# Kernel optimization log

Measured on AMD Instinct MI355X. Metric: run time of the kernel, lower is better.

The kernel has to match this reference:

```python
import jax, jax.numpy as jnp
import numpy as np

B, S, HID = 2, 2048, 2048
H, HKV, D = 16, 4, 128        # num_heads, num_kv_heads, head_dim
G = H // HKV                   # GQA group size
CLIP = 8.0                     # clip_qkv
THETA = 10000.0                # rope_theta_within_seq
N_SEQS = 8                     # max_num_sequences


def setup_inputs() -> dict:
    key = jax.random.key(0)
    ks = jax.random.split(key, 6)
    hidden_states = jax.random.normal(ks[0], (B, S, HID), dtype=jnp.float32)
    within_seq_position_ids = jnp.broadcast_to(jnp.arange(S, dtype=jnp.int64), (B, S))
    global_position_ids = jnp.broadcast_to(jnp.arange(S, dtype=jnp.int64), (B, S))
    sequence_ids = jnp.sort(jax.random.randint(ks[1], (B, S), 0, N_SEQS, dtype=jnp.int64), axis=-1)
    scale = 0.02
    Wq = jax.random.normal(ks[2], (H * D, HID), dtype=jnp.float32) * scale
    Wk = jax.random.normal(ks[3], (HKV * D, HID), dtype=jnp.float32) * scale
    Wv = jax.random.normal(ks[4], (HKV * D, HID), dtype=jnp.float32) * scale
    Wo = jax.random.normal(ks[5], (HID, H * D), dtype=jnp.float32) * scale
    return {"hidden_states": hidden_states,
            "within_seq_position_ids": within_seq_position_ids,
            "global_position_ids": global_position_ids,
            "sequence_ids": sequence_ids,
            "Wq": Wq, "Wk": Wk, "Wv": Wv, "Wo": Wo}


def _rotate_half(x):
    x1, x2 = jnp.split(x, 2, axis=-1)
    return jnp.concatenate((-x2, x1), axis=-1)


def _rope_cos_sin(position_ids, dtype):
    # inv_freq: [D/2]
    inv_freq = THETA ** (-(jnp.arange(0, D, 2, dtype=jnp.float32) / D))
    angles = position_ids.astype(jnp.float32)[..., None] * inv_freq  # [B,S,D/2]
    angles = jnp.concatenate((angles, angles), axis=-1)              # [B,S,D]
    # unsqueeze head dim -> [B,S,1,D]
    return jnp.cos(angles)[:, :, None, :].astype(dtype), jnp.sin(angles)[:, :, None, :].astype(dtype)


def reference(hidden_states, within_seq_position_ids, global_position_ids, sequence_ids, Wq, Wk, Wv, Wo):
    b, s, _ = hidden_states.shape
    q = (hidden_states @ Wq.T).reshape(b, s, H, D)
    k = (hidden_states @ Wk.T).reshape(b, s, HKV, D)
    v = (hidden_states @ Wv.T).reshape(b, s, HKV, D)
    # clip_qkv
    q = jnp.clip(q, -CLIP, CLIP)
    k = jnp.clip(k, -CLIP, CLIP)
    v = jnp.clip(v, -CLIP, CLIP)
    # RoPE (within_seq layer -> within_seq_position_ids)
    cos, sin = _rope_cos_sin(within_seq_position_ids, q.dtype)
    q = q * cos + _rotate_half(q) * sin
    k = k * cos + _rotate_half(k) * sin
    # GQA: group queries by kv head instead of materializing repeat_kv
    q = q.transpose(0, 2, 1, 3).reshape(b, HKV, G, s, D)  # [B,HKV,G,S,D]
    k = k.transpose(0, 2, 1, 3)                            # [B,HKV,S,D]
    v = v.transpose(0, 2, 1, 3)
    scores = jnp.einsum('bhgqd,bhkd->bhgqk', q, k) / jnp.sqrt(jnp.asarray(D, q.dtype))
    # block-diagonal (same sequence) causal mask
    qi = jnp.arange(s)
    causal = qi[:, None] >= qi[None, :]                    # [S,S]
    same_seq = sequence_ids[:, :, None] == sequence_ids[:, None, :]  # [B,S,S]
    mask = (causal[None] & same_seq)[:, None, None, :, :]  # [B,1,1,S,S]
    scores = jnp.where(mask, scores, jnp.finfo(scores.dtype).min)
    attn = jax.nn.softmax(scores, axis=-1)
    out = jnp.einsum('bhgqk,bhkd->bhgqd', attn, v)         # [B,HKV,G,S,D]
    out = out.reshape(b, H, s, D).transpose(0, 2, 1, 3).reshape(b, s, H * D)
    return out @ Wo.T
```

## Files before the change

### kernel.cpp

```cpp
#include <hip/hip_runtime.h>
#include <hip/hip_bf16.h>

typedef __hip_bfloat16 bf16;
typedef __attribute__((ext_vector_type(8))) short bf16x8;
typedef __attribute__((ext_vector_type(4))) float f32x4;

#define MFMA_BF16(a, b, c) __builtin_amdgcn_mfma_f32_16x16x32_bf16((a), (b), (c), 0, 0, 0)

#define B_   2
#define S_   2048
#define HID_ 2048
#define H_   16
#define HKV_ 4
#define D_   128

#define GLOAD_LDS(gptr, lptr) \
  __builtin_amdgcn_global_load_lds((const __attribute__((address_space(1))) void*)(gptr), \
                                   (__attribute__((address_space(3))) void*)(lptr), 16, 0, 0)

template <int N>
__device__ __forceinline__ void vmw() {
  if constexpr (N == 0)      asm volatile("s_waitcnt vmcnt(0)" ::: "memory");
  else if constexpr (N == 4) asm volatile("s_waitcnt vmcnt(4)" ::: "memory");
  else if constexpr (N == 5) asm volatile("s_waitcnt vmcnt(5)" ::: "memory");
  else                       asm volatile("s_waitcnt vmcnt(6)" ::: "memory");
}

__device__ __forceinline__ void blk_barrier() {
  __builtin_amdgcn_sched_barrier(0);
  __builtin_amdgcn_s_barrier();
  __builtin_amdgcn_sched_barrier(0);
}

__global__ void cvt_all(const float* __restrict__ hidden, const float* __restrict__ Wq,
                        const float* __restrict__ Wk, const float* __restrict__ Wv,
                        const float* __restrict__ Wo,
                        bf16* __restrict__ Xb, bf16* __restrict__ Wqkv, bf16* __restrict__ Wob) {
  long long i4 = (long long)blockIdx.x * 256 + threadIdx.x;
  const float* src; bf16* dst; long long off;
  if (i4 < 2097152)      { src = hidden; dst = Xb;             off = i4; }
  else if (i4 < 3145728) { src = Wq;     dst = Wqkv;           off = i4 - 2097152; }
  else if (i4 < 3407872) { src = Wk;     dst = Wqkv + 4194304; off = i4 - 3145728; }
  else if (i4 < 3670016) { src = Wv;     dst = Wqkv + 5242880; off = i4 - 3407872; }
  else                   { src = Wo;     dst = Wob;            off = i4 - 3670016; }
  float4 v = *reinterpret_cast<const float4*>(src + off * 4);
  alignas(8) bf16 t[4];
  t[0] = __float2bfloat16(v.x);
  t[1] = __float2bfloat16(v.y);
  t[2] = __float2bfloat16(v.z);
  t[3] = __float2bfloat16(v.w);
  *reinterpret_cast<short4*>(dst + off * 4) = *reinterpret_cast<const short4*>(t);
}

__global__ void seq_start(const int* __restrict__ seq, int* __restrict__ sstart) {
  int t = blockIdx.x * 256 + threadIdx.x;
  int b = t >> 11, s = t & (S_ - 1);
  const int* sb = seq + b * S_;
  int sid = sb[s];
  int lo = 0, hi = s;
  while (lo < hi) {
    int mid = (lo + hi) >> 1;
    if (sb[mid] < sid) lo = mid + 1; else hi = mid;
  }
  sstart[t] = lo;
}

template <int BM, int BN, int OUT_BF16>
__global__ __launch_bounds__(512, 2) void gemm8p(const bf16* __restrict__ A,
                                                 const bf16* __restrict__ Bw,
                                                 void* __restrict__ Cout,
                                                 int M, int N, int K) {
  constexpr int MR = BM / 32;
  constexpr int NR = BN / 64;
  constexpr int LA = BM / 128;
  constexpr int QD = NR + 2;

  __shared__ bf16 As[2][2][BM * 32];
  __shared__ bf16 Bs[2][BN * 64];

  const int tid  = threadIdx.x;
  const int lane = tid & 63;
  const int w    = tid >> 6;
  const int wr   = w >> 2;
  const int wc   = w & 3;
  const int ln15 = lane & 15, g = lane >> 4;

  const int nwg = gridDim.x;
  int bid = blockIdx.x;
  bid = (bid & 7) * (nwg >> 3) + (bid >> 3);
  const int nbn = N / BN;
  const int m0 = (bid / nbn) * BM;
  const int n0 = (bid % nbn) * BN;

  f32x4 acc[MR][NR] = {};

  auto stageA = [&](int db, int kh, int t) {
    int kc = t * 64 + kh * 32;
#pragma unroll
    for (int r = 0; r < LA; r++) {
      int sIdx = r * 512 + tid;
      int row = sIdx >> 2;
      int ss = (sIdx & 3) ^ ((row >> 1) & 3);
      GLOAD_LDS(A + (size_t)(m0 + row) * K + kc + ss * 8, &As[db][kh][(r * 512 + w * 64) * 8]);
    }
  };
  auto stageB = [&](int db, int t) {
#pragma unroll
    for (int r = 0; r < NR; r++) {
      int sIdx = r * 512 + tid;
      int row = sIdx >> 3;
      int cs = (sIdx & 7) ^ (row & 7);
      GLOAD_LDS(Bw + (size_t)(n0 + row) * K + t * 64 + cs * 8, &Bs[db][(size_t)(r * 512 + w * 64) * 8]);
    }
  };

  bf16x8 af[4], bfr[NR];
  auto rdA = [&](int db, int kh, int mb) {
#pragma unroll
    for (int m = 0; m < 4; m++) {
      int row = wr * (BM / 2) + (mb + m) * 16 + ln15;
      af[m] = *reinterpret_cast<const bf16x8*>(&As[db][kh][row * 32 + ((g ^ ((row >> 1) & 3)) << 3)]);
    }
  };
  auto rdB = [&](int db, int kh) {
#pragma unroll
    for (int n = 0; n < NR; n++) {
      int row = wc * (BN / 4) + n * 16 + ln15;
      int sl = ((kh << 2) + g) ^ (row & 7);
      bfr[n] = *reinterpret_cast<const bf16x8*>(&Bs[db][row * 64 + sl * 8]);
    }
  };
  auto MF = [&](int mb) {
    __builtin_amdgcn_s_setprio(1);
#pragma unroll
    for (int m = 0; m < 4; m++)
#pragma unroll
      for (int n = 0; n < NR; n++)
        acc[mb + m][n] = MFMA_BF16(af[m], bfr[n], acc[mb + m][n]);
    __builtin_amdgcn_s_setprio(0);
  };

  const int NT = K >> 6;

  stageA(0, 0, 0);
  stageA(0, 1, 0);
  stageB(0, 0);
  stageA(1, 0, 1);
  stageB(1, 1);
  vmw<QD>();
  blk_barrier();

  for (int T = 0; T < NT; ++T) {
    const int db = T & 1, dn = db ^ 1;

    rdA(db, 0, 0); rdB(db, 0);
    if (T + 1 < NT) stageA(dn, 1, T + 1);
    blk_barrier(); MF(0); blk_barrier();
    rdA(db, 0, 4);
    blk_barrier(); MF(4); blk_barrier();
    rdA(db, 1, 0); rdB(db, 1);
    if (T + 2 < NT) stageA(db, 0, T + 2);
    blk_barrier(); MF(0); blk_barrier();
    rdA(db, 1, 4);
    if (T + 2 < NT) stageB(db, T + 2);
    if (T + 1 < NT) {
      if (T == NT - 2) vmw<0>(); else vmw<QD>();
    }
    blk_barrier(); MF(4); blk_barrier();
  }

#pragma unroll
  for (int m = 0; m < MR; m++)
#pragma unroll
    for (int n = 0; n < NR; n++)
#pragma unroll
      for (int r = 0; r < 4; r++) {
        int row = m0 + wr * (BM / 2) + m * 16 + g * 4 + r;
        int col = n0 + wc * (BN / 4) + n * 16 + ln15;
        if constexpr (OUT_BF16) {
          ((bf16*)Cout)[(size_t)row * N + col] = __float2bfloat16(acc[m][n][r]);
        } else {
          ((float*)Cout)[(size_t)row * N + col] = acc[m][n][r];
        }
      }
}

__global__ __launch_bounds__(256) void qkv_post(const bf16* __restrict__ QKV,
                                                const int* __restrict__ wpos,
                                                bf16* __restrict__ Qs,
                                                bf16* __restrict__ Ks,
                                                bf16* __restrict__ Vt) {
  const int row = blockIdx.x;
  const int b = row >> 11, s = row & (S_ - 1);
  const int t = threadIdx.x;
  const bf16* R = QKV + (size_t)row * 3072;
  const float pos = (float)wpos[row];
  const float kln = 0.14391156831212787f;
  const float qscale = 0.08838834764831845f;

  for (int p = t; p < 1024; p += 256) {
    int h = p >> 6, i = p & 63;
    float ang = pos * expf(-(float)i * kln);
    float sn, cs;
    sincosf(ang, &sn, &cs);
    float x1 = __bfloat162float(R[h * 128 + i]);
    float x2 = __bfloat162float(R[h * 128 + 64 + i]);
    x1 = fminf(fmaxf(x1, -8.f), 8.f);
    x2 = fminf(fmaxf(x2, -8.f), 8.f);
    float y1 = (x1 * cs - x2 * sn) * qscale;
    float y2 = (x2 * cs + x1 * sn) * qscale;
    size_t qb = ((size_t)(b * H_ + h) * S_ + s) * D_;
    Qs[qb + i]      = __float2bfloat16(y1);
    Qs[qb + 64 + i] = __float2bfloat16(y2);
  }
  {
    int kh = t >> 6, i = t & 63;
    float ang = pos * expf(-(float)i * kln);
    float sn, cs;
    sincosf(ang, &sn, &cs);
    float x1 = __bfloat162float(R[2048 + kh * 128 + i]);
    float x2 = __bfloat162float(R[2048 + kh * 128 + 64 + i]);
    x1 = fminf(fmaxf(x1, -8.f), 8.f);
    x2 = fminf(fmaxf(x2, -8.f), 8.f);
    float y1 = x1 * cs - x2 * sn;
    float y2 = x2 * cs + x1 * sn;
    size_t kb = ((size_t)(b * HKV_ + kh) * S_ + s) * D_;
    Ks[kb + i]      = __float2bfloat16(y1);
    Ks[kb + 64 + i] = __float2bfloat16(y2);
  }
  for (int e = t; e < 512; e += 256) {
    int kh = e >> 7, d = e & 127;
    float x = __bfloat162float(R[2560 + e]);
    x = fminf(fmaxf(x, -8.f), 8.f);
    Vt[((size_t)(b * HKV_ + kh) * D_ + d) * S_ + s] = __float2bfloat16(x);
  }
}

__global__ __launch_bounds__(256) void attn_fwd(const bf16* __restrict__ Qs,
                                                const bf16* __restrict__ Ks,
                                                const bf16* __restrict__ Vt,
                                                const int* __restrict__ sstart,
                                                bf16* __restrict__ att) {
  __shared__ bf16 Kl[2][32 * 128];
  __shared__ bf16 Vl[2][128 * 32];
  __shared__ bf16 Plds[4][16 * 32];

  const int tid = threadIdx.x;
  const int lane = tid & 63, w = tid >> 6;
  const int ln15 = lane & 15, g = lane >> 4;

  const int wg = ((blockIdx.x & 7) << 7) | (blockIdx.x >> 3);
  const int qt  = wg & 127;
  const int kvh = (wg >> 7) & 3;
  const int b   = wg >> 9;
  const int h   = kvh * 4 + w;
  const int q0  = qt * 16;
  const int qi  = q0 + ln15;

  const bf16* Qrow = Qs + ((size_t)(b * H_ + h) * S_ + qi) * D_;
  bf16x8 qf[4];
#pragma unroll
  for (int c = 0; c < 4; c++)
    qf[c] = *reinterpret_cast<const bf16x8*>(Qrow + c * 32 + g * 8);

  const int sQ = sstart[b * S_ + qi];
  const int kstart = __builtin_amdgcn_readfirstlane(__shfl(sQ, 0));
  const int kend = q0 + 15;

  const bf16* Kb = Ks + (size_t)(b * HKV_ + kvh) * S_ * D_;
  const bf16* Vb = Vt + (size_t)(b * HKV_ + kvh) * D_ * S_;

  auto stage = [&](int buf, int kb) {
#pragma unroll
    for (int p = 0; p < 2; p++) {
      int slot = p * 256 + tid;
      int row = slot >> 4;
      int cs = (slot & 15) ^ (row & 15);
      int gr = min(kb + row, S_ - 1);
      GLOAD_LDS(Kb + (size_t)gr * D_ + cs * 8, &Kl[buf][(p * 256 + w * 64) * 8]);
    }
#pragma unroll
    for (int p = 0; p < 2; p++) {
      int slot = p * 256 + tid;
      int d = slot >> 2, c = slot & 3;
      int cs = c ^ (d & 3);
      int gcol = min(kb + cs * 8, S_ - 8);
      GLOAD_LDS(Vb + (size_t)d * S_ + gcol, &Vl[buf][(p * 256 + w * 64) * 8]);
    }
  };

  float m = -1e30f, lsum = 0.f;
  f32x4 o[8] = {};

  stage(0, kstart);
  int buf = 0;
  for (int kb = kstart; kb <= kend; kb += 32) {
    __syncthreads();
    if (kb + 32 <= kend) stage(buf ^ 1, kb + 32);

    bf16x8 kf0[4], kf1[4];
#pragma unroll
    for (int c = 0; c < 4; c++) {
      kf0[c] = *reinterpret_cast<const bf16x8*>(&Kl[buf][ln15 * 128 + (((c * 4 + g) ^ ln15) << 3)]);
      kf1[c] = *reinterpret_cast<const bf16x8*>(&Kl[buf][(16 + ln15) * 128 + (((c * 4 + g) ^ ln15) << 3)]);
    }
    f32x4 s0 = {0.f, 0.f, 0.f, 0.f}, s1 = {0.f, 0.f, 0.f, 0.f};
#pragma unroll
    for (int c = 0; c < 4; c++) {
      s0 = MFMA_BF16(kf0[c], qf[c], s0);
      s1 = MFMA_BF16(kf1[c], qf[c], s1);
    }

    float sc[8];
    float tmax = -1e30f;
#pragma unroll
    for (int r = 0; r < 4; r++) {
      int k0i = kb + g * 4 + r;
      int k1i = k0i + 16;
      float x0 = (k0i >= sQ && k0i <= qi) ? s0[r] : -1e30f;
      float x1 = (k1i >= sQ && k1i <= qi) ? s1[r] : -1e30f;
      sc[r] = x0;
      sc[4 + r] = x1;
      tmax = fmaxf(tmax, fmaxf(x0, x1));
    }
    tmax = fmaxf(tmax, __shfl_xor(tmax, 16));
    tmax = fmaxf(tmax, __shfl_xor(tmax, 32));
    float mn  = fmaxf(m, tmax);
    float fac = __expf(m - mn);
    float ps = 0.f;
    alignas(16) bf16 pb[8];
#pragma unroll
    for (int i2 = 0; i2 < 8; i2++) {
      float p = (sc[i2] < -1e29f) ? 0.f : __expf(sc[i2] - mn);
      ps += p;
      pb[i2] = __float2bfloat16(p);
    }
    ps += __shfl_xor(ps, 16);
    ps += __shfl_xor(ps, 32);
    lsum = lsum * fac + ps;
    m = mn;
#pragma unroll
    for (int t2 = 0; t2 < 8; t2++) o[t2] *= fac;

    *reinterpret_cast<short4*>(&Plds[w][ln15 * 32 + g * 4])      = *reinterpret_cast<const short4*>(&pb[0]);
    *reinterpret_cast<short4*>(&Plds[w][ln15 * 32 + 16 + g * 4]) = *reinterpret_cast<const short4*>(&pb[4]);
    __builtin_amdgcn_wave_barrier();
    bf16x8 pf = *reinterpret_cast<const bf16x8*>(&Plds[w][ln15 * 32 + g * 8]);

#pragma unroll
    for (int t2 = 0; t2 < 8; t2++) {
      int d = t2 * 16 + ln15;
      bf16x8 vf = *reinterpret_cast<const bf16x8*>(&Vl[buf][d * 32 + ((g ^ (ln15 & 3)) << 3)]);
      o[t2] = MFMA_BF16(vf, pf, o[t2]);
    }
    __builtin_amdgcn_wave_barrier();
    buf ^= 1;
  }

  float inv = 1.f / lsum;
#pragma unroll
  for (int t2 = 0; t2 < 8; t2++)
#pragma unroll
    for (int r = 0; r < 4; r++) {
      int d = t2 * 16 + g * 4 + r;
      att[((size_t)(b * S_ + qi)) * (H_ * D_) + h * D_ + d] = __float2bfloat16(o[t2][r] * inv);
    }
}

extern "C" void kernel_launch(void* const* d_in, const int* in_sizes, int n_in,
                              void* d_out, int out_size, void* d_ws, size_t ws_size,
                              hipStream_t stream) {
  const float* hidden = (const float*)d_in[0];
  const int* wpos = (const int*)d_in[1];
  const int* seq = (const int*)d_in[3];
  const float* Wq = (const float*)d_in[4];
  const float* Wk = (const float*)d_in[5];
  const float* Wv = (const float*)d_in[6];
  const float* Wo = (const float*)d_in[7];

  char* ws = (char*)d_ws;
  bf16* Xb   = (bf16*)(ws);
  bf16* Wqkv = (bf16*)(ws + 16777216);
  bf16* Wob  = (bf16*)(ws + 29360128);
  bf16* QKVb = (bf16*)(ws + 37748736);
  bf16* Ksb  = (bf16*)(ws + 62914560);
  bf16* Vtb  = (bf16*)(ws + 67108864);
  int*  sst  = (int*)(ws + 71303168);
  bf16* Qsb  = Xb;
  bf16* attb = QKVb;

  cvt_all<<<dim3(18432), dim3(256), 0, stream>>>(hidden, Wq, Wk, Wv, Wo, Xb, Wqkv, Wob);
  seq_start<<<dim3(32), dim3(256), 0, stream>>>(seq, sst);

  gemm8p<256, 192, 1><<<dim3(256), dim3(512), 0, stream>>>(Xb, Wqkv, (void*)QKVb, 4096, 3072, 2048);

  qkv_post<<<dim3(4096), dim3(256), 0, stream>>>(QKVb, wpos, Qsb, Ksb, Vtb);

  attn_fwd<<<dim3(1024), dim3(256), 0, stream>>>(Qsb, Ksb, Vtb, sst, attb);

  gemm8p<256, 128, 0><<<dim3(256), dim3(512), 0, stream>>>(attb, Wob, d_out, 4096, 2048, 2048);
}
```

Before: 174.7 us.

## Switch GEMM inner loop to 32x32x16 bf16 MFMA with configurable warp grid

Rewrites the projection GEMM kernel to use 32x32x16 MFMA instructions instead of 16x16x32, with a templated wave layout (4x2 for QKV, 2x4 for output projection). Larger MFMA tiles mean fewer LDS fragment reads per FLOP and higher per-instruction throughput. Fragment indexing, swizzled LDS reads and the epilogue store layout are adapted to the 32x32 accumulator format. The trade-off is more accumulator registers per wave and a less coalesced epilogue.

```diff
diff --git a/kernel.cpp b/kernel.cpp
--- a/kernel.cpp
+++ b/kernel.cpp
@@ -4,8 +4,10 @@
 typedef __hip_bfloat16 bf16;
 typedef __attribute__((ext_vector_type(8))) short bf16x8;
 typedef __attribute__((ext_vector_type(4))) float f32x4;
+typedef __attribute__((ext_vector_type(16))) float f32x16;
 
 #define MFMA_BF16(a, b, c) __builtin_amdgcn_mfma_f32_16x16x32_bf16((a), (b), (c), 0, 0, 0)
+#define MFMA32(a, b, c)    __builtin_amdgcn_mfma_f32_32x32x16_bf16((a), (b), (c), 0, 0, 0)
 
 #define B_   2
 #define S_   2048
@@ -65,15 +67,20 @@
   sstart[t] = lo;
 }
 
-template <int BM, int BN, int OUT_BF16>
-__global__ __launch_bounds__(512, 2) void gemm8p(const bf16* __restrict__ A,
+template <int BM, int BN, int WM, int OUT_BF16>
+__global__ __launch_bounds__(512, 2) void gemm32(const bf16* __restrict__ A,
                                                  const bf16* __restrict__ Bw,
                                                  void* __restrict__ Cout,
                                                  int M, int N, int K) {
-  constexpr int MR = BM / 32;
-  constexpr int NR = BN / 64;
-  constexpr int LA = BM / 128;
-  constexpr int QD = NR + 2;
+  constexpr int WN  = 8 / WM;
+  constexpr int PWM = BM / WM;
+  constexpr int PWN = BN / WN;
+  constexpr int MR  = PWM / 32;
+  constexpr int NR  = PWN / 32;
+  constexpr int MH  = MR / 2;
+  constexpr int NB  = BN / 64;
+  constexpr int LA  = BM / 128;
+  constexpr int QD  = NB + 2;
 
   __shared__ bf16 As[2][2][BM * 32];
   __shared__ bf16 Bs[2][BN * 64];
@@ -81,9 +88,10 @@
   const int tid  = threadIdx.x;
   const int lane = tid & 63;
   const int w    = tid >> 6;
-  const int wr   = w >> 2;
-  const int wc   = w & 3;
-  const int ln15 = lane & 15, g = lane >> 4;
+  const int wrow = w / WN;
+  const int wcol = w % WN;
+  const int l31  = lane & 31;
+  const int khi  = lane >> 5;
 
   const int nwg = gridDim.x;
   int bid = blockIdx.x;
@@ -92,7 +100,8 @@
   const int m0 = (bid / nbn) * BM;
   const int n0 = (bid % nbn) * BN;
 
-  f32x4 acc[MR][NR] = {};
+  f32x16 acc[MR][NR] = {};
+  bf16x8 af[2][MH], bfr[2][NR];
 
   auto stageA = [&](int db, int kh, int t) {
     int kc = t * 64 + kh * 32;
@@ -106,7 +115,7 @@
   };
   auto stageB = [&](int db, int t) {
 #pragma unroll
-    for (int r = 0; r < NR; r++) {
+    for (int r = 0; r < NB; r++) {
       int sIdx = r * 512 + tid;
       int row = sIdx >> 3;
       int cs = (sIdx & 7) ^ (row & 7);
@@ -114,29 +123,35 @@
     }
   };
 
-  bf16x8 af[4], bfr[NR];
-  auto rdA = [&](int db, int kh, int mb) {
-#pragma unroll
-    for (int m = 0; m < 4; m++) {
-      int row = wr * (BM / 2) + (mb + m) * 16 + ln15;
-      af[m] = *reinterpret_cast<const bf16x8*>(&As[db][kh][row * 32 + ((g ^ ((row >> 1) & 3)) << 3)]);
-    }
+  auto rdA = [&](int db, int kh, int mh) {
+#pragma unroll
+    for (int s = 0; s < 2; s++)
+#pragma unroll
+      for (int m = 0; m < MH; m++) {
+        int row = wrow * PWM + (mh * MH + m) * 32 + l31;
+        int slot = ((s << 1) + khi) ^ ((row >> 1) & 3);
+        af[s][m] = *reinterpret_cast<const bf16x8*>(&As[db][kh][row * 32 + slot * 8]);
+      }
   };
   auto rdB = [&](int db, int kh) {
 #pragma unroll
-    for (int n = 0; n < NR; n++) {
-      int row = wc * (BN / 4) + n * 16 + ln15;
-      int sl = ((kh << 2) + g) ^ (row & 7);
-      bfr[n] = *reinterpret_cast<const bf16x8*>(&Bs[db][row * 64 + sl * 8]);
-    }
-  };
-  auto MF = [&](int mb) {
+    for (int s = 0; s < 2; s++)
+#pragma unroll
+      for (int n = 0; n < NR; n++) {
+        int col = wcol * PWN + n * 32 + l31;
+        int sl = ((kh << 2) + (s << 1) + khi) ^ (col & 7);
+        bfr[s][n] = *reinterpret_cast<const bf16x8*>(&Bs[db][col * 64 + sl * 8]);
+      }
+  };
+  auto MF = [&](int mh) {
     __builtin_amdgcn_s_setprio(1);
 #pragma unroll
-    for (int m = 0; m < 4; m++)
-#pragma unroll
-      for (int n = 0; n < NR; n++)
-        acc[mb + m][n] = MFMA_BF16(af[m], bfr[n], acc[mb + m][n]);
+    for (int s = 0; s < 2; s++)
+#pragma unroll
+      for (int m = 0; m < MH; m++)
+#pragma unroll
+        for (int n = 0; n < NR; n++)
+          acc[mh * MH + m][n] = MFMA32(af[s][m], bfr[s][n], acc[mh * MH + m][n]);
     __builtin_amdgcn_s_setprio(0);
   };
 
@@ -156,31 +171,31 @@
     rdA(db, 0, 0); rdB(db, 0);
     if (T + 1 < NT) stageA(dn, 1, T + 1);
     blk_barrier(); MF(0); blk_barrier();
-    rdA(db, 0, 4);
-    blk_barrier(); MF(4); blk_barrier();
+    rdA(db, 0, 1);
+    blk_barrier(); MF(1); blk_barrier();
     rdA(db, 1, 0); rdB(db, 1);
     if (T + 2 < NT) stageA(db, 0, T + 2);
     blk_barrier(); MF(0); blk_barrier();
-    rdA(db, 1, 4);
+    rdA(db, 1, 1);
     if (T + 2 < NT) stageB(db, T + 2);
     if (T + 1 < NT) {
       if (T == NT - 2) vmw<0>(); else vmw<QD>();
     }
-    blk_barrier(); MF(4); blk_barrier();
-  }
-
-#pragma unroll
-  for (int m = 0; m < MR; m++)
-#pragma unroll
-    for (int n = 0; n < NR; n++)
-#pragma unroll
-      for (int r = 0; r < 4; r++) {
-        int row = m0 + wr * (BM / 2) + m * 16 + g * 4 + r;
-        int col = n0 + wc * (BN / 4) + n * 16 + ln15;
+    blk_barrier(); MF(1); blk_barrier();
+  }
+
+#pragma unroll
+  for (int mr = 0; mr < MR; mr++)
+#pragma unroll
+    for (int nc = 0; nc < NR; nc++)
+#pragma unroll
+      for (int reg = 0; reg < 16; reg++) {
+        int row = m0 + wrow * PWM + mr * 32 + (reg & 3) + ((reg >> 2) << 3) + (khi << 2);
+        int col = n0 + wcol * PWN + nc * 32 + l31;
         if constexpr (OUT_BF16) {
-          ((bf16*)Cout)[(size_t)row * N + col] = __float2bfloat16(acc[m][n][r]);
+          ((bf16*)Cout)[(size_t)row * N + col] = __float2bfloat16(acc[mr][nc][reg]);
         } else {
-          ((float*)Cout)[(size_t)row * N + col] = acc[m][n][r];
+          ((float*)Cout)[(size_t)row * N + col] = acc[mr][nc][reg];
         }
       }
 }
@@ -392,11 +407,11 @@
   cvt_all<<<dim3(18432), dim3(256), 0, stream>>>(hidden, Wq, Wk, Wv, Wo, Xb, Wqkv, Wob);
   seq_start<<<dim3(32), dim3(256), 0, stream>>>(seq, sst);
 
-  gemm8p<256, 192, 1><<<dim3(256), dim3(512), 0, stream>>>(Xb, Wqkv, (void*)QKVb, 4096, 3072, 2048);
+  gemm32<256, 192, 4, 1><<<dim3(256), dim3(512), 0, stream>>>(Xb, Wqkv, (void*)QKVb, 4096, 3072, 2048);
 
   qkv_post<<<dim3(4096), dim3(256), 0, stream>>>(QKVb, wpos, Qsb, Ksb, Vtb);
 
   attn_fwd<<<dim3(1024), dim3(256), 0, stream>>>(Qsb, Ksb, Vtb, sst, attb);
 
-  gemm8p<256, 128, 0><<<dim3(256), dim3(512), 0, stream>>>(attb, Wob, d_out, 4096, 2048, 2048);
-}
+  gemm32<256, 128, 2, 0><<<dim3(256), dim3(512), 0, stream>>>(attb, Wob, d_out, 4096, 2048, 2048);
+}
```

Result: slower. 181.0 us (+3.6%).

## Process two 16-row query tiles per wave in attention to reuse K/V tiles

Applied to the files above, without the earlier changes.

Each attention wave now handles 32 query rows as two 16-row tiles, so every K/V tile staged in LDS feeds twice as many MFMAs, and the grid is halved to 512 blocks. This cuts redundant K/V global loads and LDS traffic per query. In exchange it raises register pressure, roughly doubling accumulators and Q fragments, gives fewer blocks for load balancing, and adds masked work on the diagonal tile.

```diff
diff --git a/kernel.cpp b/kernel.cpp
--- a/kernel.cpp
+++ b/kernel.cpp
@@ -156,11 +156,14 @@
     rdA(db, 0, 0); rdB(db, 0);
     if (T + 1 < NT) stageA(dn, 1, T + 1);
     blk_barrier(); MF(0); blk_barrier();
+
     rdA(db, 0, 4);
     blk_barrier(); MF(4); blk_barrier();
+
     rdA(db, 1, 0); rdB(db, 1);
     if (T + 2 < NT) stageA(db, 0, T + 2);
     blk_barrier(); MF(0); blk_barrier();
+
     rdA(db, 1, 4);
     if (T + 2 < NT) stageB(db, T + 2);
     if (T + 1 < NT) {
@@ -243,29 +246,33 @@
                                                 bf16* __restrict__ att) {
   __shared__ bf16 Kl[2][32 * 128];
   __shared__ bf16 Vl[2][128 * 32];
-  __shared__ bf16 Plds[4][16 * 32];
+  __shared__ bf16 Plds[4][2][16 * 32];
 
   const int tid = threadIdx.x;
   const int lane = tid & 63, w = tid >> 6;
   const int ln15 = lane & 15, g = lane >> 4;
 
-  const int wg = ((blockIdx.x & 7) << 7) | (blockIdx.x >> 3);
-  const int qt  = wg & 127;
-  const int kvh = (wg >> 7) & 3;
-  const int b   = wg >> 9;
+  const int wg = ((blockIdx.x & 7) << 6) | (blockIdx.x >> 3);
+  const int qt  = wg & 63;
+  const int kvh = (wg >> 6) & 3;
+  const int b   = wg >> 8;
   const int h   = kvh * 4 + w;
-  const int q0  = qt * 16;
-  const int qi  = q0 + ln15;
-
-  const bf16* Qrow = Qs + ((size_t)(b * H_ + h) * S_ + qi) * D_;
-  bf16x8 qf[4];
-#pragma unroll
-  for (int c = 0; c < 4; c++)
-    qf[c] = *reinterpret_cast<const bf16x8*>(Qrow + c * 32 + g * 8);
-
-  const int sQ = sstart[b * S_ + qi];
-  const int kstart = __builtin_amdgcn_readfirstlane(__shfl(sQ, 0));
-  const int kend = q0 + 15;
+  const int q0  = qt * 32;
+  const int qa  = q0 + ln15;
+  const int qb  = q0 + 16 + ln15;
+
+  const bf16* Qbase = Qs + (size_t)(b * H_ + h) * S_ * D_;
+  bf16x8 qfa[4], qfb[4];
+#pragma unroll
+  for (int c = 0; c < 4; c++) {
+    qfa[c] = *reinterpret_cast<const bf16x8*>(Qbase + (size_t)qa * D_ + c * 32 + g * 8);
+    qfb[c] = *reinterpret_cast<const bf16x8*>(Qbase + (size_t)qb * D_ + c * 32 + g * 8);
+  }
+
+  const int sQa = sstart[b * S_ + qa];
+  const int sQb = sstart[b * S_ + qb];
+  const int kstart = __builtin_amdgcn_readfirstlane(__shfl(sQa, 0));
+  const int kend = q0 + 31;
 
   const bf16* Kb = Ks + (size_t)(b * HKV_ + kvh) * S_ * D_;
   const bf16* Vb = Vt + (size_t)(b * HKV_ + kvh) * D_ * S_;
@@ -289,28 +296,11 @@
     }
   };
 
-  float m = -1e30f, lsum = 0.f;
-  f32x4 o[8] = {};
-
-  stage(0, kstart);
-  int buf = 0;
-  for (int kb = kstart; kb <= kend; kb += 32) {
-    __syncthreads();
-    if (kb + 32 <= kend) stage(buf ^ 1, kb + 32);
-
-    bf16x8 kf0[4], kf1[4];
-#pragma unroll
-    for (int c = 0; c < 4; c++) {
-      kf0[c] = *reinterpret_cast<const bf16x8*>(&Kl[buf][ln15 * 128 + (((c * 4 + g) ^ ln15) << 3)]);
-      kf1[c] = *reinterpret_cast<const bf16x8*>(&Kl[buf][(16 + ln15) * 128 + (((c * 4 + g) ^ ln15) << 3)]);
-    }
-    f32x4 s0 = {0.f, 0.f, 0.f, 0.f}, s1 = {0.f, 0.f, 0.f, 0.f};
-#pragma unroll
-    for (int c = 0; c < 4; c++) {
-      s0 = MFMA_BF16(kf0[c], qf[c], s0);
-      s1 = MFMA_BF16(kf1[c], qf[c], s1);
-    }
-
+  float ma = -1e30f, la = 0.f, mb = -1e30f, lb = 0.f;
+  f32x4 oa[8] = {}, ob[8] = {};
+
+  auto softmax = [&](const f32x4& s0, const f32x4& s1, int qi, int sQ, int kb,
+                     float& m, float& lsum, f32x4 (&o)[8], bf16* pdst) {
     float sc[8];
     float tmax = -1e30f;
 #pragma unroll
@@ -341,29 +331,57 @@
     m = mn;
 #pragma unroll
     for (int t2 = 0; t2 < 8; t2++) o[t2] *= fac;
-
-    *reinterpret_cast<short4*>(&Plds[w][ln15 * 32 + g * 4])      = *reinterpret_cast<const short4*>(&pb[0]);
-    *reinterpret_cast<short4*>(&Plds[w][ln15 * 32 + 16 + g * 4]) = *reinterpret_cast<const short4*>(&pb[4]);
+    *reinterpret_cast<short4*>(pdst + ln15 * 32 + g * 4)      = *reinterpret_cast<const short4*>(&pb[0]);
+    *reinterpret_cast<short4*>(pdst + ln15 * 32 + 16 + g * 4) = *reinterpret_cast<const short4*>(&pb[4]);
+  };
+
+  stage(0, kstart);
+  int buf = 0;
+  for (int kb = kstart; kb <= kend; kb += 32) {
+    __syncthreads();
+    if (kb + 32 <= kend) stage(buf ^ 1, kb + 32);
+
+    bf16x8 kf0[4], kf1[4];
+#pragma unroll
+    for (int c = 0; c < 4; c++) {
+      kf0[c] = *reinterpret_cast<const bf16x8*>(&Kl[buf][ln15 * 128 + (((c * 4 + g) ^ ln15) << 3)]);
+      kf1[c] = *reinterpret_cast<const bf16x8*>(&Kl[buf][(16 + ln15) * 128 + (((c * 4 + g) ^ ln15) << 3)]);
+    }
+    f32x4 sa0 = {0.f, 0.f, 0.f, 0.f}, sa1 = sa0, sb0 = sa0, sb1 = sa0;
+#pragma unroll
+    for (int c = 0; c < 4; c++) {
+      sa0 = MFMA_BF16(kf0[c], qfa[c], sa0);
+      sa1 = MFMA_BF16(kf1[c], qfa[c], sa1);
+      sb0 = MFMA_BF16(kf0[c], qfb[c], sb0);
+      sb1 = MFMA_BF16(kf1[c], qfb[c], sb1);
+    }
+
+    softmax(sa0, sa1, qa, sQa, kb, ma, la, oa, &Plds[w][0][0]);
+    softmax(sb0, sb1, qb, sQb, kb, mb, lb, ob, &Plds[w][1][0]);
     __builtin_amdgcn_wave_barrier();
-    bf16x8 pf = *reinterpret_cast<const bf16x8*>(&Plds[w][ln15 * 32 + g * 8]);
+    bf16x8 pfa = *reinterpret_cast<const bf16x8*>(&Plds[w][0][ln15 * 32 + g * 8]);
+    bf16x8 pfb = *reinterpret_cast<const bf16x8*>(&Plds[w][1][ln15 * 32 + g * 8]);
 
 #pragma unroll
     for (int t2 = 0; t2 < 8; t2++) {
       int d = t2 * 16 + ln15;
       bf16x8 vf = *reinterpret_cast<const bf16x8*>(&Vl[buf][d * 32 + ((g ^ (ln15 & 3)) << 3)]);
-      o[t2] = MFMA_BF16(vf, pf, o[t2]);
+      oa[t2] = MFMA_BF16(vf, pfa, oa[t2]);
+      ob[t2] = MFMA_BF16(vf, pfb, ob[t2]);
     }
     __builtin_amdgcn_wave_barrier();
     buf ^= 1;
   }
 
-  float inv = 1.f / lsum;
+  float inva = 1.f / la;
+  float invb = 1.f / lb;
 #pragma unroll
   for (int t2 = 0; t2 < 8; t2++)
 #pragma unroll
     for (int r = 0; r < 4; r++) {
       int d = t2 * 16 + g * 4 + r;
-      att[((size_t)(b * S_ + qi)) * (H_ * D_) + h * D_ + d] = __float2bfloat16(o[t2][r] * inv);
+      att[((size_t)(b * S_ + qa)) * (H_ * D_) + h * D_ + d] = __float2bfloat16(oa[t2][r] * inva);
+      att[((size_t)(b * S_ + qb)) * (H_ * D_) + h * D_ + d] = __float2bfloat16(ob[t2][r] * invb);
     }
 }
 
@@ -396,7 +414,7 @@
 
   qkv_post<<<dim3(4096), dim3(256), 0, stream>>>(QKVb, wpos, Qsb, Ksb, Vtb);
 
-  attn_fwd<<<dim3(1024), dim3(256), 0, stream>>>(Qsb, Ksb, Vtb, sst, attb);
+  attn_fwd<<<dim3(512), dim3(256), 0, stream>>>(Qsb, Ksb, Vtb, sst, attb);
 
   gemm8p<256, 128, 0><<<dim3(256), dim3(512), 0, stream>>>(attb, Wob, d_out, 4096, 2048, 2048);
 }
```

Result: no change. 175.1 us (+0.2%).
